# Performance work log

Hardware: AMD Instinct MI355X
Metric: run time of the kernel (lower is better)

The kernel has to match this reference:

```python
import jax, jax.numpy as jnp
import numpy as np

H, W = 4096, 4096
KH, KW = 15, 15


def setup_inputs() -> dict:
    key = jax.random.key(0)
    k1, k2 = jax.random.split(key)
    x = jax.random.normal(k1, (H, W), dtype=jnp.float32)
    weight = jax.random.normal(k2, (KH, KW), dtype=jnp.float32)
    bias = jnp.zeros((1,), dtype=jnp.float32)
    return {"x": x, "weight": weight, "bias": bias}


def reference(x, weight, bias):
    # corr2d: valid cross-correlation of 2D x with 2D kernel, output [H-KH+1, W-KW+1]
    # lax conv with NCHW/OIHW layout computes cross-correlation (no kernel flip),
    # identical to the torch per-pixel slice-multiply-sum loop.
    out = jax.lax.conv_general_dilated(
        x[None, None, :, :],            # [1,1,H,W]
        weight[None, None, :, :],       # [1,1,KH,KW]
        window_strides=(1, 1),
        padding="VALID",
    )[0, 0]                             # [H-KH+1, W-KW+1]
    return out + bias  # bias is shape [1], broadcasts like torch
```

## Files before the change

### kernel.cpp

```cpp
#include <hip/hip_runtime.h>


#define HIN 4096
#define WIN 4096
#define KH 15
#define KW 15
#define OH (HIN - KH + 1)
#define OW (WIN - KW + 1)

#define BX 64
#define BY 64
#define XROWS (BY + KH - 1)
#define XCOLS 80
#define LDSW 88
#define BTAB (XROWS * LDSW)
#define NSH (BTAB + 15 * 64 * 8)

typedef short bf16x8 __attribute__((ext_vector_type(8)));
typedef float f32x4  __attribute__((ext_vector_type(4)));

static __device__ inline short f2bf(float f) {
    unsigned u = __float_as_uint(f);
    u += 0x7fffu + ((u >> 16) & 1u);
    return (short)(u >> 16);
}

__global__ __launch_bounds__(256)
void conv2d_mfma(const float* __restrict__ x,
                 const float* __restrict__ w,
                 const float* __restrict__ bias,
                 float* __restrict__ out) {
    __shared__ short lds[NSH];

    const int tid = threadIdx.x;
    const int ox0 = blockIdx.x * BX;
    const int oy0 = blockIdx.y * BY;

    for (int f = tid; f < XROWS * (XCOLS / 4); f += 256) {
        const int r  = f / (XCOLS / 4);
        const int c4 = (f - r * (XCOLS / 4)) * 4;
        int gy = oy0 + r;
        if (gy > HIN - 1) gy = HIN - 1;
        const int gx = ox0 + c4;
        float4 v;
        if (gx + 3 <= WIN - 1) {
            v = *reinterpret_cast<const float4*>(&x[(size_t)gy * WIN + gx]);
        } else {
            const float* row = &x[(size_t)gy * WIN];
            const int x0 = (gx + 0 > WIN - 1) ? WIN - 1 : gx + 0;
            const int x1 = (gx + 1 > WIN - 1) ? WIN - 1 : gx + 1;
            const int x2 = (gx + 2 > WIN - 1) ? WIN - 1 : gx + 2;
            const int x3 = (gx + 3 > WIN - 1) ? WIN - 1 : gx + 3;
            v = make_float4(row[x0], row[x1], row[x2], row[x3]);
        }
        short4 s;
        s.x = f2bf(v.x); s.y = f2bf(v.y); s.z = f2bf(v.z); s.w = f2bf(v.w);
        *reinterpret_cast<short4*>(&lds[r * LDSW + c4]) = s;
    }

    for (int e = tid; e < 15 * 64; e += 256) {
        const int kh = e >> 6;
        const int L  = e & 63;
        const int n  = L & 15;
        const int q  = L >> 4;
        bf16x8 bv;
#pragma unroll
        for (int j = 0; j < 8; ++j) {
            const int d = q * 8 + j - n;
            bv[j] = (d >= 0 && d < KW) ? f2bf(w[kh * KW + d]) : (short)0;
        }
        *reinterpret_cast<bf16x8*>(&lds[BTAB + e * 8]) = bv;
    }
    __syncthreads();

    const int lane = tid & 63;
    const int wv   = tid >> 6;
    const int m    = lane & 15;
    const int q    = lane >> 4;

    bf16x8 B[KH];
#pragma unroll
    for (int kh = 0; kh < KH; ++kh)
        B[kh] = *reinterpret_cast<const bf16x8*>(&lds[BTAB + (kh * 64 + lane) * 8]);

    f32x4 acc[4];
#pragma unroll
    for (int t = 0; t < 4; ++t) acc[t] = (f32x4){0.f, 0.f, 0.f, 0.f};

    const short* abase = &lds[(wv * 16 + m) * LDSW + q * 8];
#pragma unroll
    for (int kh = 0; kh < KH; ++kh) {
#pragma unroll
        for (int t = 0; t < 4; ++t) {
            const bf16x8 a =
                *reinterpret_cast<const bf16x8*>(abase + kh * LDSW + t * 16);
            acc[t] = __builtin_amdgcn_mfma_f32_16x16x32_bf16(a, B[kh], acc[t], 0, 0, 0);
        }
    }

    const float b0 = bias[0];
    const int row0 = oy0 + wv * 16 + q * 4;
#pragma unroll
    for (int t = 0; t < 4; ++t) {
        const int col = ox0 + t * 16 + m;
        if (col < OW) {
#pragma unroll
            for (int r = 0; r < 4; ++r) {
                const int row = row0 + r;
                if (row < OH)
                    out[(size_t)row * OW + col] = acc[t][r] + b0;
            }
        }
    }
}

extern "C" void kernel_launch(void* const* d_in, const int* in_sizes, int n_in,
                              void* d_out, int out_size, void* d_ws, size_t ws_size,
                              hipStream_t stream) {
    const float* x    = (const float*)d_in[0];
    const float* w    = (const float*)d_in[1];
    const float* bias = (const float*)d_in[2];
    float* out        = (float*)d_out;

    dim3 grid((OW + BX - 1) / BX, (OH + BY - 1) / BY);
    dim3 block(256);
    conv2d_mfma<<<grid, block, 0, stream>>>(x, w, bias, out);
}
```

Measured before the change: 154.9 us.

## Precompute banded weight table in separate kernel and batch interior tile loads

Moves construction of the banded bf16 weight table out of every block into a small pre-kernel that writes it to workspace, and the main kernel now reads it from global memory (L2-cached) per kh instead of from LDS. This cuts LDS usage and per-block setup work. It also adds a fast path for interior tiles that issues all float4 loads before converting and storing, to raise memory-level parallelism, and sets launch bounds for 8 blocks per CU. In exchange it adds an extra kernel launch and global loads inside the MFMA loop.

```diff
diff --git a/kernel.cpp b/kernel.cpp
--- a/kernel.cpp
+++ b/kernel.cpp
@@ -13,8 +13,9 @@
 #define XROWS (BY + KH - 1)
 #define XCOLS 80
 #define LDSW 88
-#define BTAB (XROWS * LDSW)
-#define NSH (BTAB + 15 * 64 * 8)
+#define NSH (XROWS * LDSW)
+#define NB4 (XCOLS / 4)
+#define NITEM (XROWS * NB4)
 
 typedef short bf16x8 __attribute__((ext_vector_type(8)));
 typedef float f32x4  __attribute__((ext_vector_type(4)));
@@ -25,9 +26,25 @@
     return (short)(u >> 16);
 }
 
-__global__ __launch_bounds__(256)
+__global__ void conv2d_btab(const float* __restrict__ w, short* __restrict__ btab) {
+    const int e = blockIdx.x * 256 + threadIdx.x;
+    if (e >= KH * 64) return;
+    const int kh = e >> 6;
+    const int L  = e & 63;
+    const int n  = L & 15;
+    const int q  = L >> 4;
+    bf16x8 bv;
+#pragma unroll
+    for (int j = 0; j < 8; ++j) {
+        const int d = q * 8 + j - n;
+        bv[j] = (d >= 0 && d < KW) ? f2bf(w[kh * KW + d]) : (short)0;
+    }
+    *reinterpret_cast<bf16x8*>(&btab[(size_t)e * 8]) = bv;
+}
+
+__global__ __launch_bounds__(256, 8)
 void conv2d_mfma(const float* __restrict__ x,
-                 const float* __restrict__ w,
+                 const short* __restrict__ btab,
                  const float* __restrict__ bias,
                  float* __restrict__ out) {
     __shared__ short lds[NSH];
@@ -36,40 +53,51 @@
     const int ox0 = blockIdx.x * BX;
     const int oy0 = blockIdx.y * BY;
 
-    for (int f = tid; f < XROWS * (XCOLS / 4); f += 256) {
-        const int r  = f / (XCOLS / 4);
-        const int c4 = (f - r * (XCOLS / 4)) * 4;
-        int gy = oy0 + r;
-        if (gy > HIN - 1) gy = HIN - 1;
-        const int gx = ox0 + c4;
-        float4 v;
-        if (gx + 3 <= WIN - 1) {
-            v = *reinterpret_cast<const float4*>(&x[(size_t)gy * WIN + gx]);
-        } else {
-            const float* row = &x[(size_t)gy * WIN];
-            const int x0 = (gx + 0 > WIN - 1) ? WIN - 1 : gx + 0;
-            const int x1 = (gx + 1 > WIN - 1) ? WIN - 1 : gx + 1;
-            const int x2 = (gx + 2 > WIN - 1) ? WIN - 1 : gx + 2;
-            const int x3 = (gx + 3 > WIN - 1) ? WIN - 1 : gx + 3;
-            v = make_float4(row[x0], row[x1], row[x2], row[x3]);
+    if (ox0 + XCOLS <= WIN && oy0 + XROWS <= HIN) {
+        float4 v[7];
+#pragma unroll
+        for (int i = 0; i < 7; ++i) {
+            const int f = tid + 256 * i;
+            if (f < NITEM) {
+                const int r  = f / NB4;
+                const int c4 = (f - r * NB4) * 4;
+                v[i] = *reinterpret_cast<const float4*>(&x[(size_t)(oy0 + r) * WIN + ox0 + c4]);
+            }
         }
-        short4 s;
-        s.x = f2bf(v.x); s.y = f2bf(v.y); s.z = f2bf(v.z); s.w = f2bf(v.w);
-        *reinterpret_cast<short4*>(&lds[r * LDSW + c4]) = s;
-    }
-
-    for (int e = tid; e < 15 * 64; e += 256) {
-        const int kh = e >> 6;
-        const int L  = e & 63;
-        const int n  = L & 15;
-        const int q  = L >> 4;
-        bf16x8 bv;
 #pragma unroll
-        for (int j = 0; j < 8; ++j) {
-            const int d = q * 8 + j - n;
-            bv[j] = (d >= 0 && d < KW) ? f2bf(w[kh * KW + d]) : (short)0;
+        for (int i = 0; i < 7; ++i) {
+            const int f = tid + 256 * i;
+            if (f < NITEM) {
+                const int r  = f / NB4;
+                const int c4 = (f - r * NB4) * 4;
+                short4 s;
+                s.x = f2bf(v[i].x); s.y = f2bf(v[i].y);
+                s.z = f2bf(v[i].z); s.w = f2bf(v[i].w);
+                *reinterpret_cast<short4*>(&lds[r * LDSW + c4]) = s;
+            }
         }
-        *reinterpret_cast<bf16x8*>(&lds[BTAB + e * 8]) = bv;
+    } else {
+        for (int f = tid; f < NITEM; f += 256) {
+            const int r  = f / NB4;
+            const int c4 = (f - r * NB4) * 4;
+            int gy = oy0 + r;
+            if (gy > HIN - 1) gy = HIN - 1;
+            const int gx = ox0 + c4;
+            float4 v;
+            if (gx + 3 <= WIN - 1) {
+                v = *reinterpret_cast<const float4*>(&x[(size_t)gy * WIN + gx]);
+            } else {
+                const float* row = &x[(size_t)gy * WIN];
+                const int x0 = (gx + 0 > WIN - 1) ? WIN - 1 : gx + 0;
+                const int x1 = (gx + 1 > WIN - 1) ? WIN - 1 : gx + 1;
+                const int x2 = (gx + 2 > WIN - 1) ? WIN - 1 : gx + 2;
+                const int x3 = (gx + 3 > WIN - 1) ? WIN - 1 : gx + 3;
+                v = make_float4(row[x0], row[x1], row[x2], row[x3]);
+            }
+            short4 s;
+            s.x = f2bf(v.x); s.y = f2bf(v.y); s.z = f2bf(v.z); s.w = f2bf(v.w);
+            *reinterpret_cast<short4*>(&lds[r * LDSW + c4]) = s;
+        }
     }
     __syncthreads();
 
@@ -78,23 +106,20 @@
     const int m    = lane & 15;
     const int q    = lane >> 4;
 
-    bf16x8 B[KH];
-#pragma unroll
-    for (int kh = 0; kh < KH; ++kh)
-        B[kh] = *reinterpret_cast<const bf16x8*>(&lds[BTAB + (kh * 64 + lane) * 8]);
-
     f32x4 acc[4];
 #pragma unroll
     for (int t = 0; t < 4; ++t) acc[t] = (f32x4){0.f, 0.f, 0.f, 0.f};
 
-    const short* abase = &lds[(wv * 16 + m) * LDSW + q * 8];
+    const short*  abase = &lds[(wv * 16 + m) * LDSW + q * 8];
+    const bf16x8* bt    = reinterpret_cast<const bf16x8*>(btab) + lane;
 #pragma unroll
     for (int kh = 0; kh < KH; ++kh) {
+        const bf16x8 b = bt[kh * 64];
 #pragma unroll
         for (int t = 0; t < 4; ++t) {
             const bf16x8 a =
                 *reinterpret_cast<const bf16x8*>(abase + kh * LDSW + t * 16);
-            acc[t] = __builtin_amdgcn_mfma_f32_16x16x32_bf16(a, B[kh], acc[t], 0, 0, 0);
+            acc[t] = __builtin_amdgcn_mfma_f32_16x16x32_bf16(a, b, acc[t], 0, 0, 0);
         }
     }
 
@@ -121,8 +146,11 @@
     const float* w    = (const float*)d_in[1];
     const float* bias = (const float*)d_in[2];
     float* out        = (float*)d_out;
+    short* btab       = (short*)d_ws;
+
+    conv2d_btab<<<dim3((KH * 64 + 255) / 256), dim3(256), 0, stream>>>(w, btab);
 
     dim3 grid((OW + BX - 1) / BX, (OH + BY - 1) / BY);
     dim3 block(256);
-    conv2d_mfma<<<grid, block, 0, stream>>>(x, w, bias, out);
+    conv2d_mfma<<<grid, block, 0, stream>>>(x, btab, bias, out);
 }
```

Measured after the change: 138.2 us. 1.12x faster.
